# Kernel tuning notes

Measured on AMD Instinct MI355X. Metric: run time of the kernel, lower is better.

The kernel has to match this reference:

```python
import jax, jax.numpy as jnp
import numpy as np
from math import sqrt

B, L, S, H, E = 4, 2048, 2048, 16, 64


def setup_inputs() -> dict:
    key = jax.random.key(0)
    kq, kk, kv = jax.random.split(key, 3)
    queries = jax.random.normal(kq, (B, L, H, E), dtype=jnp.float32)
    keys = jax.random.normal(kk, (B, S, H, E), dtype=jnp.float32)
    values = jax.random.normal(kv, (B, S, H, E), dtype=jnp.float32)
    # causal mask: True where attention is disallowed (upper triangle, excl diag)
    causal = jnp.triu(jnp.ones((L, S), dtype=jnp.bool_), k=1)
    attention_mask = jnp.broadcast_to(causal[None, None, :, :], (B, 1, L, S))
    return {"queries": queries, "keys": keys, "values": values,
            "attention_mask": attention_mask}


def reference(queries, keys, values, attention_mask):
    E_ = queries.shape[-1]
    scale = 1.0 / sqrt(E_)
    # [B,H,L,S] full score matrix (the quadratic intermediate of naive attention)
    scores = jnp.einsum('blhe,bshe->bhls', queries, keys)
    scores = jnp.where(attention_mask, -jnp.inf, scores)
    A = jnp.nan_to_num(jax.nn.softmax(scale * scores, axis=-1))
    V = jnp.einsum('bhls,bshd->blhd', A, values)
    return V
```

## Files before the change

kernel.cpp:

```cpp
#include <hip/hip_runtime.h>
#include <cmath>

#define B_ 4
#define L_ 2048
#define S_ 2048
#define H_ 16
#define E_ 64
#define SCALE2 0.18033688011112042f

typedef __attribute__((ext_vector_type(4))) float f32x4;
typedef __attribute__((ext_vector_type(8))) __bf16 bf16x8;
typedef __attribute__((ext_vector_type(8))) unsigned short ushort8;
union FragU { ushort8 u; bf16x8 b; unsigned int d[4]; };

__device__ __forceinline__ unsigned short f2bf(float f) {
    unsigned int u = __float_as_uint(f);
    return (unsigned short)((u + 0x7FFFu + ((u >> 16) & 1u)) >> 16);
}

__device__ __forceinline__ unsigned int pack_bf(float hi, float lo) {
    return __builtin_amdgcn_perm(__float_as_uint(hi), __float_as_uint(lo),
                                 0x07060302u);
}

__device__ __forceinline__ void gload_lds16(const void* g, void* l) {
    __builtin_amdgcn_global_load_lds(
        (const __attribute__((address_space(1))) void*)g,
        (__attribute__((address_space(3))) void*)l, 16, 0, 0);
}

__global__ __launch_bounds__(256) void conv_k(const float* __restrict__ K,
                                              unsigned short* __restrict__ Kbf) {
    const int idx = blockIdx.x * 256 + threadIdx.x;
    const int j   = idx & 7;
    const int row = idx >> 3;
    const int s   = row & (S_ - 1);
    const int bh  = row >> 11;
    const int h   = bh & (H_ - 1);
    const int b   = bh >> 4;
    const int jp  = j ^ (s & 7);
    const float* src = K + (((size_t)b * S_ + s) * H_ + h) * E_ + jp * 8;
    f32x4 a = *(const f32x4*)src;
    f32x4 d = *(const f32x4*)(src + 4);
    ushort8 u;
    u[0]=f2bf(a[0]); u[1]=f2bf(a[1]); u[2]=f2bf(a[2]); u[3]=f2bf(a[3]);
    u[4]=f2bf(d[0]); u[5]=f2bf(d[1]); u[6]=f2bf(d[2]); u[7]=f2bf(d[3]);
    *(ushort8*)(Kbf + (size_t)row * E_ + j * 8) = u;
}

__global__ __launch_bounds__(256) void conv_v(const float* __restrict__ V,
                                              unsigned short* __restrict__ Vt) {
    __shared__ unsigned short t[64 * 65];
    const int tid  = threadIdx.x;
    const int sblk = blockIdx.x & 31;
    const int h    = (blockIdx.x >> 5) & 15;
    const int b    = blockIdx.x >> 9;
    const int s0   = sblk * 64;
    for (int i = 0; i < 4; ++i) {
        const int c = tid + i * 256;
        const int sr = c >> 4, e0 = (c & 15) * 4;
        f32x4 a = *(const f32x4*)(V + (((size_t)b * S_ + s0 + sr) * H_ + h) * E_ + e0);
        t[sr * 65 + e0 + 0] = f2bf(a[0]);
        t[sr * 65 + e0 + 1] = f2bf(a[1]);
        t[sr * 65 + e0 + 2] = f2bf(a[2]);
        t[sr * 65 + e0 + 3] = f2bf(a[3]);
    }
    __syncthreads();
    for (int i = 0; i < 2; ++i) {
        const int c  = tid + i * 256;
        const int e  = c >> 3, cc = c & 7;
        const int q  = cc >> 1, half = cc & 1;
        ushort8 u;
        for (int j = 0; j < 8; ++j) {
            const int d = j >> 2, r = j & 3;
            const int key = (2 * half + d) * 16 + q * 4 + r;
            u[j] = t[key * 65 + e];
        }
        *(ushort8*)(Vt + ((size_t)(b * H_ + h) * E_ + e) * S_ + s0
                    + (cc ^ (e & 7)) * 8) = u;
    }
}

template <bool PRE>
__global__ __launch_bounds__(256, 4) void fattn_kernel(
    const float* __restrict__ Q, const unsigned short* __restrict__ Kbf,
    const unsigned short* __restrict__ Vt, const float* __restrict__ Kf,
    const float* __restrict__ Vf, float* __restrict__ Out)
{
    const int tid  = threadIdx.x;
    const int wave = tid >> 6;
    const int lane = tid & 63;
    const int ln   = lane & 15;
    const int quad = lane >> 4;
    const int qtile = (blockIdx.x + blockIdx.y + 4 * blockIdx.z) & 15;
    const int h = blockIdx.y;
    const int b = blockIdx.z;
    const int q0 = qtile * 128;
    const int qw = q0 + wave * 32;
    const int p7 = ln & 7;

    __shared__ __align__(16) unsigned short ldsK[2][64 * 64];
    __shared__ __align__(16) unsigned short ldsV[2][64 * 64];

    FragU qf[2][2];
    #pragma unroll
    for (int g = 0; g < 2; ++g) {
        const float* qp = Q + (((size_t)b * L_ + (qw + g * 16 + ln)) * H_ + h) * E_;
        #pragma unroll
        for (int c = 0; c < 2; ++c) {
            const int e0 = c * 32 + quad * 8;
            f32x4 lo = *(const f32x4*)(qp + e0);
            f32x4 hi = *(const f32x4*)(qp + e0 + 4);
            ushort8 u;
            u[0]=f2bf(lo[0]*SCALE2); u[1]=f2bf(lo[1]*SCALE2);
            u[2]=f2bf(lo[2]*SCALE2); u[3]=f2bf(lo[3]*SCALE2);
            u[4]=f2bf(hi[0]*SCALE2); u[5]=f2bf(hi[1]*SCALE2);
            u[6]=f2bf(hi[2]*SCALE2); u[7]=f2bf(hi[3]*SCALE2);
            qf[g][c].u = u;
        }
    }

    f32x4 o[2][4];
    #pragma unroll
    for (int g = 0; g < 2; ++g)
        #pragma unroll
        for (int et = 0; et < 4; ++et) o[g][et] = f32x4{0.f, 0.f, 0.f, 0.f};
    float lsum[2] = {0.f, 0.f};

    const unsigned short* kbh = Kbf + (size_t)(b * H_ + h) * S_ * E_;
    const unsigned short* vbh = Vt  + (size_t)(b * H_ + h) * E_ * S_;
    const float* kf32 = Kf + (((size_t)b * S_) * H_ + h) * E_;
    const float* vf32 = Vf + (((size_t)b * S_) * H_ + h) * E_;

    auto STAGE = [&](int bsel, int kt2) {
        const int k0s = kt2 * 64;
        if constexpr (PRE) {
            const unsigned short* ktb = kbh + (size_t)k0s * E_;
            const unsigned short* vtb = vbh + k0s;
            #pragma unroll
            for (int i = 0; i < 2; ++i) {
                const int slot0 = wave * 128 + i * 64;
                gload_lds16(ktb + (size_t)(slot0 + lane) * 8,
                            &ldsK[bsel][slot0 * 8]);
            }
            #pragma unroll
            for (int i = 0; i < 2; ++i) {
                const int slot0 = wave * 128 + i * 64;
                const int slot  = slot0 + lane;
                const int e = slot >> 3, lc = slot & 7;
                gload_lds16(vtb + (size_t)e * S_ + lc * 8,
                            &ldsV[bsel][slot0 * 8]);
            }
        } else {
            #pragma unroll
            for (int i = 0; i < 2; ++i) {
                const int c = tid + i * 256;
                const int key = c >> 3, j = c & 7, jp = j ^ (key & 7);
                const float* src = kf32 + (size_t)(k0s + key) * (H_ * E_) + jp * 8;
                f32x4 a = *(const f32x4*)src, d = *(const f32x4*)(src + 4);
                ushort8 u;
                u[0]=f2bf(a[0]); u[1]=f2bf(a[1]); u[2]=f2bf(a[2]); u[3]=f2bf(a[3]);
                u[4]=f2bf(d[0]); u[5]=f2bf(d[1]); u[6]=f2bf(d[2]); u[7]=f2bf(d[3]);
                *(ushort8*)&ldsK[bsel][key * 64 + j * 8] = u;
            }
            #pragma unroll
            for (int i = 0; i < 2; ++i) {
                const int c = tid + i * 256;
                const int e = c >> 3, cc = c & 7;
                const int q = cc >> 1, half = cc & 1;
                ushort8 u;
                #pragma unroll
                for (int j = 0; j < 8; ++j) {
                    const int d = j >> 2, r = j & 3;
                    const int key = (2 * half + d) * 16 + q * 4 + r;
                    u[j] = f2bf(vf32[(size_t)(k0s + key) * (H_ * E_) + e]);
                }
                *(ushort8*)&ldsV[bsel][e * 64 + (cc ^ (e & 7)) * 8] = u;
            }
        }
    };

    const int ntiles = 2 * qtile + 2;
    STAGE(0, 0);
    int cur = 0;
    for (int kt = 0; kt < ntiles; ++kt) {
        const int k0 = kt * 64;
        __syncthreads();
        if (kt + 1 < ntiles) STAGE(cur ^ 1, kt + 1);

        if (k0 <= qw + 31) {
            __builtin_amdgcn_s_setprio(1);
            const unsigned short* bK = ldsK[cur];
            const unsigned short* bV = ldsV[cur];
            const bool m0 = (k0 + 63 > qw);
            const bool m1 = (k0 + 63 > qw + 16);

            FragU pf[2][2];
            #pragma unroll
            for (int n = 0; n < 4; ++n) {
                FragU kf0, kf1;
                kf0.u = *(const ushort8*)&bK[(n*16+ln)*64 + ((quad    ) ^ p7) * 8];
                kf1.u = *(const ushort8*)&bK[(n*16+ln)*64 + ((4 + quad) ^ p7) * 8];
                #pragma unroll
                for (int g = 0; g < 2; ++g) {
                    f32x4 acc = f32x4{0.f, 0.f, 0.f, 0.f};
                    acc = __builtin_amdgcn_mfma_f32_16x16x32_bf16(kf0.b, qf[g][0].b, acc, 0, 0, 0);
                    acc = __builtin_amdgcn_mfma_f32_16x16x32_bf16(kf1.b, qf[g][1].b, acc, 0, 0, 0);
                    const bool nm = g ? m1 : m0;
                    const int qrow = qw + g * 16 + ln;
                    float p[4];
                    #pragma unroll
                    for (int r = 0; r < 4; ++r) {
                        float v = __builtin_exp2f(acc[r]);
                        if (nm) {
                            const int key = k0 + n * 16 + quad * 4 + r;
                            v = (key <= qrow) ? v : 0.f;
                        }
                        p[r] = v;
                    }
                    lsum[g] += (p[0] + p[1]) + (p[2] + p[3]);
                    pf[g][n >> 1].d[(n & 1) * 2 + 0] = pack_bf(p[1], p[0]);
                    pf[g][n >> 1].d[(n & 1) * 2 + 1] = pack_bf(p[3], p[2]);
                }
            }

            #pragma unroll
            for (int et = 0; et < 4; ++et) {
                FragU vf0, vf1;
                vf0.u = *(const ushort8*)&bV[(et*16+ln)*64 + ((2*quad    ) ^ p7) * 8];
                vf1.u = *(const ushort8*)&bV[(et*16+ln)*64 + ((2*quad + 1) ^ p7) * 8];
                #pragma unroll
                for (int g = 0; g < 2; ++g) {
                    o[g][et] = __builtin_amdgcn_mfma_f32_16x16x32_bf16(pf[g][0].b, vf0.b, o[g][et], 0, 0, 0);
                    o[g][et] = __builtin_amdgcn_mfma_f32_16x16x32_bf16(pf[g][1].b, vf1.b, o[g][et], 0, 0, 0);
                }
            }
            __builtin_amdgcn_s_setprio(0);
        }
        cur ^= 1;
    }

    #pragma unroll
    for (int g = 0; g < 2; ++g) {
        float l = lsum[g];
        l += __shfl_xor(l, 16);
        l += __shfl_xor(l, 32);
        const float inv = 1.f / l;
        #pragma unroll
        for (int r = 0; r < 4; ++r) {
            const int row = quad * 4 + r;
            const float invr = __shfl(inv, row);
            float* op = Out + (((size_t)b * L_ + (qw + g * 16 + row)) * H_ + h) * E_;
            #pragma unroll
            for (int et = 0; et < 4; ++et)
                op[et * 16 + ln] = o[g][et][r] * invr;
        }
    }
}

extern "C" void kernel_launch(void* const* d_in, const int* in_sizes, int n_in,
                              void* d_out, int out_size, void* d_ws, size_t ws_size,
                              hipStream_t stream) {
    const float* Q = (const float*)d_in[0];
    const float* K = (const float*)d_in[1];
    const float* V = (const float*)d_in[2];
    float* Out = (float*)d_out;

    const size_t plane = (size_t)B_ * H_ * S_ * E_;
    unsigned short* Kbf = (unsigned short*)d_ws;
    unsigned short* Vt  = Kbf + plane;

    dim3 grid(L_ / 128, H_, B_);
    if (ws_size >= plane * 2 * sizeof(unsigned short)) {
        conv_k<<<(int)(plane / 8 / 256), 256, 0, stream>>>(K, Kbf);
        conv_v<<<B_ * H_ * (S_ / 64), 256, 0, stream>>>(V, Vt);
        fattn_kernel<true><<<grid, dim3(256), 0, stream>>>(Q, Kbf, Vt, K, V, Out);
    } else {
        fattn_kernel<false><<<grid, dim3(256), 0, stream>>>(Q, Kbf, Vt, K, V, Out);
    }
}
```

Baseline: 250.6 us.

## Triple-buffer K/V staging, compute row sums via MFMA, and reorder grid

```diff
diff --git a/kernel.cpp b/kernel.cpp
--- a/kernel.cpp
+++ b/kernel.cpp
@@ -92,15 +92,15 @@
     const int lane = tid & 63;
     const int ln   = lane & 15;
     const int quad = lane >> 4;
-    const int qtile = (blockIdx.x + blockIdx.y + 4 * blockIdx.z) & 15;
-    const int h = blockIdx.y;
+    const int h = blockIdx.x;
     const int b = blockIdx.z;
+    const int qtile = (blockIdx.y + blockIdx.x + 4 * blockIdx.z) & 15;
     const int q0 = qtile * 128;
     const int qw = q0 + wave * 32;
     const int p7 = ln & 7;
 
-    __shared__ __align__(16) unsigned short ldsK[2][64 * 64];
-    __shared__ __align__(16) unsigned short ldsV[2][64 * 64];
+    __shared__ __align__(16) unsigned short ldsK[3][64 * 64];
+    __shared__ __align__(16) unsigned short ldsV[3][64 * 64];
 
     FragU qf[2][2];
     #pragma unroll
@@ -120,12 +120,18 @@
         }
     }
 
+    FragU onef;
+    #pragma unroll
+    for (int j = 0; j < 8; ++j) onef.u[j] = 0x3F80;
+
     f32x4 o[2][4];
     #pragma unroll
     for (int g = 0; g < 2; ++g)
         #pragma unroll
         for (int et = 0; et < 4; ++et) o[g][et] = f32x4{0.f, 0.f, 0.f, 0.f};
-    float lsum[2] = {0.f, 0.f};
+    f32x4 lacc[2];
+    lacc[0] = f32x4{0.f, 0.f, 0.f, 0.f};
+    lacc[1] = f32x4{0.f, 0.f, 0.f, 0.f};
 
     const unsigned short* kbh = Kbf + (size_t)(b * H_ + h) * S_ * E_;
     const unsigned short* vbh = Vt  + (size_t)(b * H_ + h) * E_ * S_;
@@ -182,12 +188,21 @@
 
     const int ntiles = 2 * qtile + 2;
     STAGE(0, 0);
+    STAGE(1, 1);
     int cur = 0;
     for (int kt = 0; kt < ntiles; ++kt) {
+        if (kt + 1 < ntiles)
+            asm volatile("s_waitcnt vmcnt(4) lgkmcnt(0)" ::: "memory");
+        else
+            asm volatile("s_waitcnt vmcnt(0) lgkmcnt(0)" ::: "memory");
+        __builtin_amdgcn_s_barrier();
+        __builtin_amdgcn_sched_barrier(0);
+        if (kt + 2 < ntiles) {
+            int sb = cur + 2; if (sb >= 3) sb -= 3;
+            STAGE(sb, kt + 2);
+        }
+
         const int k0 = kt * 64;
-        __syncthreads();
-        if (kt + 1 < ntiles) STAGE(cur ^ 1, kt + 1);
-
         if (k0 <= qw + 31) {
             __builtin_amdgcn_s_setprio(1);
             const unsigned short* bK = ldsK[cur];
@@ -218,12 +233,16 @@
                         }
                         p[r] = v;
                     }
-                    lsum[g] += (p[0] + p[1]) + (p[2] + p[3]);
                     pf[g][n >> 1].d[(n & 1) * 2 + 0] = pack_bf(p[1], p[0]);
                     pf[g][n >> 1].d[(n & 1) * 2 + 1] = pack_bf(p[3], p[2]);
                 }
             }
 
+            #pragma unroll
+            for (int g = 0; g < 2; ++g) {
+                lacc[g] = __builtin_amdgcn_mfma_f32_16x16x32_bf16(pf[g][0].b, onef.b, lacc[g], 0, 0, 0);
+                lacc[g] = __builtin_amdgcn_mfma_f32_16x16x32_bf16(pf[g][1].b, onef.b, lacc[g], 0, 0, 0);
+            }
             #pragma unroll
             for (int et = 0; et < 4; ++et) {
                 FragU vf0, vf1;
@@ -237,20 +256,15 @@
             }
             __builtin_amdgcn_s_setprio(0);
         }
-        cur ^= 1;
+        ++cur; if (cur == 3) cur = 0;
     }
 
     #pragma unroll
     for (int g = 0; g < 2; ++g) {
-        float l = lsum[g];
-        l += __shfl_xor(l, 16);
-        l += __shfl_xor(l, 32);
-        const float inv = 1.f / l;
         #pragma unroll
         for (int r = 0; r < 4; ++r) {
-            const int row = quad * 4 + r;
-            const float invr = __shfl(inv, row);
-            float* op = Out + (((size_t)b * L_ + (qw + g * 16 + row)) * H_ + h) * E_;
+            const float invr = 1.f / lacc[g][r];
+            float* op = Out + (((size_t)b * L_ + (qw + g * 16 + quad * 4 + r)) * H_ + h) * E_;
             #pragma unroll
             for (int et = 0; et < 4; ++et)
                 op[et * 16 + ln] = o[g][et][r] * invr;
@@ -270,7 +284,7 @@
     unsigned short* Kbf = (unsigned short*)d_ws;
     unsigned short* Vt  = Kbf + plane;
 
-    dim3 grid(L_ / 128, H_, B_);
+    dim3 grid(H_, L_ / 128, B_);
     if (ws_size >= plane * 2 * sizeof(unsigned short)) {
         conv_k<<<(int)(plane / 8 / 256), 256, 0, stream>>>(K, Kbf);
         conv_v<<<B_ * H_ * (S_ / 64), 256, 0, stream>>>(V, Vt);
```

Measured after the change: 259.1 us. 3.4% more time.
